# Performance work log

Measured on AMD Instinct MI355X. Metric: run time of the kernel, lower is better.

## Reference

```python
import jax, jax.numpy as jnp
import numpy as np

H = 256      # hidden_dim
D = 64       # dim_dynamic
ND = 2       # num_dynamic
PR = 7       # pooler_resolution
S = PR * PR  # 49 spatial positions
B = 4800     # N * nr_boxes
P = H * D    # num_params
EPS = 1e-5


def setup_inputs() -> dict:
    key = jax.random.key(0)
    ks = jax.random.split(key, 32)
    def w(k, shape):
        return jax.random.normal(k, shape, dtype=jnp.float32) * 0.02
    inp = {
        "pro_features": jax.random.normal(ks[0], (1, B, H), jnp.float32),
        "roi_features": jax.random.normal(ks[1], (S, B, H), jnp.float32),
        "pos_xywh": jax.random.normal(ks[2], (1, B, H), jnp.float32),
        "pos_img": jax.random.normal(ks[3], (S, B, H), jnp.float32),
        "pos_local": jax.random.uniform(ks[4], (PR, PR), jnp.float32),
        "bboxes_xywh": jax.random.uniform(ks[5], (B, 4), jnp.float32, minval=0.2, maxval=1.0),
        # dynamic_layer: H -> ND*P
        "Wd": w(ks[6], (H, ND * P)), "bd": jnp.zeros((ND * P,), jnp.float32),
        # query_scale MLP (2 layers, H->H->H)
        "Wqs1": w(ks[7], (H, H)), "bqs1": jnp.zeros((H,), jnp.float32),
        "Wqs2": w(ks[8], (H, H)), "bqs2": jnp.zeros((H,), jnp.float32),
        # ref_point_head MLP (2 layers, H->H->2)
        "Wr1": w(ks[9], (H, H)), "br1": jnp.zeros((H,), jnp.float32),
        "Wr2": w(ks[10], (H, 2)), "br2": jnp.zeros((2,), jnp.float32),
        # ca_qpos_proj / ca_kpos_proj
        "Wq": w(ks[11], (H, H)), "bq": jnp.zeros((H,), jnp.float32),
        "Wk": w(ks[12], (H, H)), "bk": jnp.zeros((H,), jnp.float32),
        # layer norms
        "g1": jnp.ones((D,), jnp.float32), "be1": jnp.zeros((D,), jnp.float32),
        "g2": jnp.ones((H,), jnp.float32), "be2": jnp.zeros((H,), jnp.float32),
        "g3": jnp.ones((H,), jnp.float32), "be3": jnp.zeros((H,), jnp.float32),
        # out_layer: (H*S) -> H
        "Wo": w(ks[13], (H * S, H)), "bo": jnp.zeros((H,), jnp.float32),
    }
    return inp


def _ln(x, g, b):
    m = jnp.mean(x, axis=-1, keepdims=True)
    v = jnp.mean((x - m) ** 2, axis=-1, keepdims=True)
    return (x - m) * jax.lax.rsqrt(v + EPS) * g + b


def reference(pro_features, roi_features, pos_xywh, pos_img, pos_local, bboxes_xywh,
              Wd, bd, Wqs1, bqs1, Wqs2, bqs2, Wr1, br1, Wr2, br2,
              Wq, bq, Wk, bk, g1, be1, g2, be2, g3, be3, Wo, bo):
    # (S,B,H) -> (B,S,H)
    features_pos = jnp.transpose(pos_img @ Wq + bq, (1, 0, 2))
    features = jnp.transpose(roi_features, (1, 0, 2))
    # dynamic parameters: (1,B,ND*P) -> (B,1,ND*P)
    parameters = jnp.transpose(pro_features @ Wd + bd, (1, 0, 2))
    # query_scale MLP
    pos_t = jax.nn.relu(pro_features @ Wqs1 + bqs1) @ Wqs2 + bqs2  # (1,B,H)
    px = pos_xywh[..., :H] * pos_t                                 # (1,B,H)
    # ref_point_head -> sigmoid
    ref = jax.nn.sigmoid(jax.nn.relu(pro_features @ Wr1 + br1) @ Wr2 + br2)  # (1,B,2)
    bb = bboxes_xywh.reshape(1, -1, 4)
    hi = px[..., H // 2:] * (ref[..., 0] / bb[..., 2])[..., None]
    lo = px[..., :H // 2] * (ref[..., 1] / bb[..., 3])[..., None]
    px = jnp.concatenate([lo, hi], axis=-1)
    # (B,1,H) * (1,S,1) -> (B,S,H)
    px = jnp.transpose(px, (1, 0, 2)) * pos_local.reshape(-1)[None, :, None]
    param1_pos = px @ Wk + bk                                      # (B,S,H)
    param1 = parameters[:, :, :P].reshape(-1, H, D)                # (B,H,D)
    param2 = parameters[:, :, P:].reshape(-1, D, H)                # (B,D,H)
    f = jnp.einsum('bsh,bhd->bsd', features, param1)               # (B,S,D)
    fp = jnp.sum(features_pos * param1_pos, axis=-1)               # (B,S)
    f = f + fp[:, :, None]
    f = jax.nn.relu(_ln(f, g1, be1))
    f = jnp.einsum('bsd,bdh->bsh', f, param2)                      # (B,S,H)
    f = jax.nn.relu(_ln(f, g2, be2))
    f = f.reshape(f.shape[0], -1) @ Wo + bo                        # (B,H)
    f = jax.nn.relu(_ln(f, g3, be3))
    return f
```

## Files before the change

### kernel.cpp

```cpp
#include <hip/hip_runtime.h>
#include <hip/hip_bf16.h>

#define HH 256
#define DD 64
#define SS 49
#define BB 4800
#define PP 16384
#define NDP 32768
#define KWO 12544
#define MPAD 4864
#define SK 8
#define KCH 1568

typedef unsigned int u32;
typedef unsigned short u16;
typedef __attribute__((ext_vector_type(8))) short bf16x8;
typedef __attribute__((ext_vector_type(4))) float f32x4;

__device__ __forceinline__ float bf2f(__hip_bfloat16 h) { return __bfloat162float(h); }

__device__ __forceinline__ void load_lds16(const void* g, void* l) {
  __builtin_amdgcn_global_load_lds(
      (const __attribute__((address_space(1))) unsigned int*)g,
      (__attribute__((address_space(3))) unsigned int*)l, 16, 0, 0);
}

__device__ __forceinline__ int nperm(int n) {
  if (n < PP) { int h = n >> 6, d = n & 63; return d * HH + h; }
  int r = n - PP; int d = r >> 8, h = r & 255; return PP + h * DD + d;
}

__device__ __forceinline__ float wave_sum64(float v) {
#pragma unroll
  for (int off = 32; off > 0; off >>= 1) v += __shfl_xor(v, off);
  return v;
}

__device__ __forceinline__ float block_sum256(float v, float* red) {
  v = wave_sum64(v);
  int w = threadIdx.x >> 6;
  if ((threadIdx.x & 63) == 0) red[w] = v;
  __syncthreads();
  float r = red[0] + red[1] + red[2] + red[3];
  __syncthreads();
  return r;
}

__global__ void k0_prep(const float* __restrict__ Wq, const float* __restrict__ bk,
                        const float* __restrict__ bq, float* __restrict__ w2c2) {
  __shared__ float red[4];
  int k = blockIdx.x, h = threadIdx.x;
  float v = Wq[k * HH + h];
  float s = block_sum256(v * bk[h], red);
  if (h == 0) w2c2[k] = s;
  if (k == 0) {
    float s2 = block_sum256(bq[h] * bk[h], red);
    if (h == 0) w2c2[HH] = s2;
  }
}

__global__ __launch_bounds__(256) void kc_w1(
    const float* __restrict__ Wqs1, const float* __restrict__ Wqs2,
    const float* __restrict__ Wr1, const float* __restrict__ Wk,
    const float* __restrict__ Wq,
    u16* __restrict__ w1t, u16* __restrict__ w2t, u16* __restrict__ wr1t,
    u16* __restrict__ wkt, u16* __restrict__ wqh) {
  int t = threadIdx.x;
  int zi = blockIdx.z;
  if (zi == 4) {
    int row = blockIdx.y * 32 + (t >> 3), col = blockIdx.x * 32 + (t & 7) * 4;
    float4 v = *(const float4*)&Wq[row * HH + col];
    union { u16 u[4]; uint2 q; } pk;
    __hip_bfloat16 hb;
    hb = __float2bfloat16(v.x); pk.u[0] = *(u16*)&hb;
    hb = __float2bfloat16(v.y); pk.u[1] = *(u16*)&hb;
    hb = __float2bfloat16(v.z); pk.u[2] = *(u16*)&hb;
    hb = __float2bfloat16(v.w); pk.u[3] = *(u16*)&hb;
    *(uint2*)&wqh[row * HH + col] = pk.q;
    return;
  }
  const float* src = (zi == 0) ? Wqs1 : (zi == 1) ? Wqs2 : (zi == 2) ? Wr1 : Wk;
  u16* dst = (zi == 0) ? w1t : (zi == 1) ? w2t : (zi == 2) ? wr1t : wkt;
  __shared__ float tile[32][33];
  int n0 = blockIdx.x * 32, k0 = blockIdx.y * 32;
  {
    int kk = t >> 3, nn = (t & 7) * 4;
    float4 v = *(const float4*)&src[(k0 + kk) * HH + n0 + nn];
    tile[kk][nn + 0] = v.x;
    tile[kk][nn + 1] = v.y;
    tile[kk][nn + 2] = v.z;
    tile[kk][nn + 3] = v.w;
  }
  __syncthreads();
  {
    int nn = t >> 3, kk = (t & 7) * 4;
    union { u16 u[4]; uint2 q; } pk;
#pragma unroll
    for (int i = 0; i < 4; ++i) {
      __hip_bfloat16 hb = __float2bfloat16(tile[kk + i][nn]);
      pk.u[i] = *(u16*)&hb;
    }
    *(uint2*)&dst[(n0 + nn) * HH + k0 + kk] = pk.q;
  }
}

__device__ __forceinline__ void g_gemm(const u16* aLb, const u16* __restrict__ Bg,
                                       int wm, int wn, int lg, int lr,
                                       f32x4 acc[2][4]) {
#pragma unroll
  for (int k0 = 0; k0 < HH; k0 += 32) {
    int colb = (k0 + (lg << 3)) << 1;
    bf16x8 af[2];
#pragma unroll
    for (int mi = 0; mi < 2; ++mi) {
      int row = wm * 32 + mi * 16 + lr;
      af[mi] = *(const bf16x8*)((const char*)aLb + (row << 9) +
                                (colb ^ ((row & 7) << 4)));
    }
    bf16x8 bfr[4];
#pragma unroll
    for (int ni = 0; ni < 4; ++ni) {
      int n = wn * 64 + ni * 16 + lr;
      bfr[ni] = *(const bf16x8*)&Bg[n * HH + k0 + (lg << 3)];
    }
#pragma unroll
    for (int mi = 0; mi < 2; ++mi)
#pragma unroll
      for (int ni = 0; ni < 4; ++ni)
        acc[mi][ni] = __builtin_amdgcn_mfma_f32_16x16x32_bf16(af[mi], bfr[ni], acc[mi][ni], 0, 0, 0);
  }
}

__device__ __forceinline__ void c_write(u16* xLb, f32x4 acc[2][4],
                                        const float* __restrict__ bias, bool dorelu,
                                        int wm, int wn, int lg, int lr) {
#pragma unroll
  for (int ni = 0; ni < 4; ++ni) {
    int col = wn * 64 + ni * 16 + lr;
    float bv = bias ? bias[col] : 0.f;
#pragma unroll
    for (int mi = 0; mi < 2; ++mi) {
#pragma unroll
      for (int j = 0; j < 4; ++j) {
        int row = wm * 32 + mi * 16 + (lg << 2) + j;
        float v = acc[mi][ni][j] + bv;
        if (dorelu) v = fmaxf(v, 0.f);
        __hip_bfloat16 hb = __float2bfloat16(v);
        *(u16*)((char*)xLb + (row << 9) + (((col << 1)) ^ ((row & 7) << 4))) = *(u16*)&hb;
      }
    }
  }
}

__global__ __launch_bounds__(512) void k1_mfma(
    const u16* __restrict__ proh, const float* __restrict__ posx,
    const float* __restrict__ bbox,
    const u16* __restrict__ w1t, const u16* __restrict__ w2t,
    const u16* __restrict__ wr1t, const u16* __restrict__ wkt,
    const u16* __restrict__ wqh,
    const float* __restrict__ bqs1, const float* __restrict__ bqs2,
    const float* __restrict__ br1, const float* __restrict__ Wr2,
    const float* __restrict__ br2, const float* __restrict__ bq,
    float* __restrict__ z, float* __restrict__ c1) {
  __shared__ u16 aL[16384];
  __shared__ u16 xL[16384];
  __shared__ float red0[512], red1[512];
  __shared__ float scLoL[64], scHiL[64];
  const int t = threadIdx.x;
  const int w = t >> 6, l = t & 63;
  const int lg = l >> 4, lr = l & 15;
  const int wm = w >> 2, wn = w & 3;
  const int m0 = blockIdx.x * 64;

#pragma unroll
  for (int i = 0; i < 4; ++i) {
    int c = i * 512 + t;
    int a = c * 16;
    int row = a >> 9, x0 = a & 511;
    int src = (m0 + row) * HH + ((x0 ^ ((row & 7) << 4)) >> 1);
    load_lds16(proh + src, (char*)aL + (size_t)(i * 512 + (w << 6)) * 16);
  }
  __syncthreads();

  {
    f32x4 acc[2][4] = {};
    g_gemm(aL, wr1t, wm, wn, lg, lr, acc);
    c_write(xL, acc, br1, true, wm, wn, lg, lr);
  }
  __syncthreads();
  {
    int row = t & 63, seg = t >> 6;
    float s0 = 0.f, s1 = 0.f;
#pragma unroll 8
    for (int hh = 0; hh < 32; ++hh) {
      int h = seg * 32 + hh;
      float rv = bf2f(*(const __hip_bfloat16*)((const char*)xL + (row << 9) +
                                               (((h << 1)) ^ ((row & 7) << 4))));
      s0 = fmaf(rv, Wr2[h * 2 + 0], s0);
      s1 = fmaf(rv, Wr2[h * 2 + 1], s1);
    }
    red0[row * 8 + seg] = s0;
    red1[row * 8 + seg] = s1;
  }
  __syncthreads();
  if (t < 64) {
    float s0 = br2[0], s1 = br2[1];
#pragma unroll
    for (int k = 0; k < 8; ++k) {
      s0 += red0[t * 8 + k];
      s1 += red1[t * 8 + k];
    }
    float r0 = 1.f / (1.f + __expf(-s0));
    float r1 = 1.f / (1.f + __expf(-s1));
    scHiL[t] = r0 / bbox[(m0 + t) * 4 + 2];
    scLoL[t] = r1 / bbox[(m0 + t) * 4 + 3];
  }
  f32x4 acc1[2][4] = {};
  g_gemm(aL, w1t, wm, wn, lg, lr, acc1);
  __syncthreads();
  c_write(xL, acc1, bqs1, true, wm, wn, lg, lr);
  __syncthreads();
  f32x4 accp[2][4] = {};
  g_gemm(xL, w2t, wm, wn, lg, lr, accp);
  __syncthreads();
#pragma unroll
  for (int ni = 0; ni < 4; ++ni) {
    int col = wn * 64 + ni * 16 + lr;
    float bv = bqs2[col];
#pragma unroll
    for (int mi = 0; mi < 2; ++mi) {
#pragma unroll
      for (int j = 0; j < 4; ++j) {
        int row = wm * 32 + mi * 16 + (lg << 2) + j;
        float pt = accp[mi][ni][j] + bv;
        float sc = (col < 128) ? scLoL[row] : scHiL[row];
        float v = posx[(m0 + row) * HH + col] * pt * sc;
        __hip_bfloat16 hb = __float2bfloat16(v);
        *(u16*)((char*)aL + (row << 9) + (((col << 1)) ^ ((row & 7) << 4))) = *(u16*)&hb;
      }
    }
  }
  __syncthreads();
  {
    f32x4 acc[2][4] = {};
    g_gemm(aL, wkt, wm, wn, lg, lr, acc);
    c_write(xL, acc, nullptr, false, wm, wn, lg, lr);
  }
  __syncthreads();
  {
    int row = t & 63, seg = t >> 6;
    float s0 = 0.f;
#pragma unroll 8
    for (int hh = 0; hh < 32; ++hh) {
      int h = seg * 32 + hh;
      float yv = bf2f(*(const __hip_bfloat16*)((const char*)xL + (row << 9) +
                                               (((h << 1)) ^ ((row & 7) << 4))));
      s0 = fmaf(yv, bq[h], s0);
    }
    red0[row * 8 + seg] = s0;
  }
  f32x4 accz[2][4] = {};
  g_gemm(xL, wqh, wm, wn, lg, lr, accz);
  __syncthreads();
  if (t < 64) {
    float s = 0.f;
#pragma unroll
    for (int k = 0; k < 8; ++k) s += red0[t * 8 + k];
    c1[m0 + t] = s;
  }
#pragma unroll
  for (int ni = 0; ni < 4; ++ni) {
    int col = wn * 64 + ni * 16 + lr;
#pragma unroll
    for (int mi = 0; mi < 2; ++mi) {
#pragma unroll
      for (int j = 0; j < 4; ++j) {
        int row = wm * 32 + mi * 16 + (lg << 2) + j;
        z[(size_t)(m0 + row) * HH + col] = accz[mi][ni][j];
      }
    }
  }
}

__global__ __launch_bounds__(256) void k2_fp(
    const float* __restrict__ posi, const float* __restrict__ posl,
    const float* __restrict__ z, const float* __restrict__ c1,
    const float* __restrict__ w2c2, float* __restrict__ fp) {
  int b = blockIdx.x, t = threadIdx.x;
  int l = t & 63, w = t >> 6;
  float4 zv = *(const float4*)&z[b * HH + l * 4];
  float4 wv = *(const float4*)&w2c2[l * 4];
  float c1b = c1[b];
  float c2 = w2c2[HH];
  for (int s = w; s < SS; s += 4) {
    float4 pi = *(const float4*)&posi[((size_t)s * BB + b) * HH + l * 4];
    float d1 = pi.x * zv.x + pi.y * zv.y + pi.z * zv.z + pi.w * zv.w;
    float d2 = pi.x * wv.x + pi.y * wv.y + pi.z * wv.z + pi.w * wv.w;
#pragma unroll
    for (int off = 32; off > 0; off >>= 1) {
      d1 += __shfl_xor(d1, off);
      d2 += __shfl_xor(d2, off);
    }
    if (l == 0) fp[b * SS + s] = posl[s] * (d1 + c1b) + d2 + c2;
  }
}

__global__ __launch_bounds__(256) void kc_pro(const float* __restrict__ pro,
                                              u16* __restrict__ proh) {
  int tg = blockIdx.x * 256 + threadIdx.x;
  int e0 = tg * 8;
  int row = e0 >> 8;
  union { u16 u[8]; uint4 v; } pk;
  if (row < BB) {
    float4 v0 = *(const float4*)&pro[e0];
    float4 v1 = *(const float4*)&pro[e0 + 4];
    float vv[8] = {v0.x, v0.y, v0.z, v0.w, v1.x, v1.y, v1.z, v1.w};
#pragma unroll
    for (int i = 0; i < 8; ++i) {
      __hip_bfloat16 hb = __float2bfloat16(vv[i]);
      pk.u[i] = *(u16*)&hb;
    }
  } else {
    pk.v = make_uint4(0, 0, 0, 0);
  }
  *(uint4*)&proh[e0] = pk.v;
}

__global__ __launch_bounds__(256) void kc_wdt(const float* __restrict__ Wd,
                                              u16* __restrict__ wdt) {
  __shared__ float tile[32][33];
  int n0 = blockIdx.x * 32;
  int k0 = blockIdx.y * 32;
  int t = threadIdx.x;
  {
    int kk = t >> 3, nn = (t & 7) * 4;
    float4 v = *(const float4*)&Wd[(size_t)(k0 + kk) * NDP + n0 + nn];
    tile[kk][nn + 0] = v.x;
    tile[kk][nn + 1] = v.y;
    tile[kk][nn + 2] = v.z;
    tile[kk][nn + 3] = v.w;
  }
  __syncthreads();
  {
    int nn = t >> 3, kk = (t & 7) * 4;
    union { u16 u[4]; uint2 v; } pk;
#pragma unroll
    for (int i = 0; i < 4; ++i) {
      __hip_bfloat16 hb = __float2bfloat16(tile[kk + i][nn]);
      pk.u[i] = *(u16*)&hb;
    }
    int np = nperm(n0 + nn);
    *(uint2*)&wdt[(size_t)np * HH + k0 + kk] = pk.v;
  }
}

__global__ void kc_bdp(const float* __restrict__ bd, float* __restrict__ bdp) {
  int n = blockIdx.x * 256 + threadIdx.x;
  bdp[nperm(n)] = bd[n];
}

__global__ __launch_bounds__(256) void kc_wot(const float* __restrict__ Wo,
                                              u16* __restrict__ wot) {
  __shared__ float tile[32][33];
  int k0 = blockIdx.x * 32;
  int n0 = blockIdx.y * 32;
  int t = threadIdx.x;
  {
    int kk = t >> 3, nn = (t & 7) * 4;
    float4 v = *(const float4*)&Wo[(size_t)(k0 + kk) * HH + n0 + nn];
    tile[kk][nn + 0] = v.x;
    tile[kk][nn + 1] = v.y;
    tile[kk][nn + 2] = v.z;
    tile[kk][nn + 3] = v.w;
  }
  __syncthreads();
  {
    int nn = t >> 3, kk = (t & 7) * 4;
    union { u16 u[4]; uint2 v; } pk;
#pragma unroll
    for (int i = 0; i < 4; ++i) {
      __hip_bfloat16 hb = __float2bfloat16(tile[kk + i][nn]);
      pk.u[i] = *(u16*)&hb;
    }
    *(uint2*)&wot[(size_t)(n0 + nn) * KWO + k0 + kk] = pk.v;
  }
}

__global__ __launch_bounds__(256) void k3_mfma(const u16* __restrict__ proh,
                                               const u16* __restrict__ wdt,
                                               const float* __restrict__ bdp,
                                               u16* __restrict__ params) {
  __shared__ char smem[32768];
  u16* Al = (u16*)smem;
  u16* Bl = (u16*)(smem + 8192);
  const int t = threadIdx.x;
  const int w = t >> 6, l = t & 63;
  const int n0 = blockIdx.x * 128;
  const int m0 = blockIdx.y * 128;
  const int wr = w >> 1, wc = w & 1;
  f32x4 acc[4][4] = {};

  for (int k0 = 0; k0 < HH; k0 += 32) {
#pragma unroll
    for (int i = 0; i < 2; ++i) {
      int c = i * 256 + t;
      int r = c >> 2, kq = (c & 3) * 8;
      int wbase = (i * 256 + (w << 6)) * 8;
      load_lds16(proh + (size_t)(m0 + r) * HH + k0 + kq, Al + wbase);
      load_lds16(wdt + (size_t)(n0 + r) * HH + k0 + kq, Bl + wbase);
    }
    __syncthreads();
    bf16x8 af[4], bfr[4];
#pragma unroll
    for (int mi = 0; mi < 4; ++mi)
      af[mi] = *(const bf16x8*)&Al[(wr * 64 + mi * 16 + (l & 15)) * 32 + (l >> 4) * 8];
#pragma unroll
    for (int ni = 0; ni < 4; ++ni)
      bfr[ni] = *(const bf16x8*)&Bl[(wc * 64 + ni * 16 + (l & 15)) * 32 + (l >> 4) * 8];
#pragma unroll
    for (int mi = 0; mi < 4; ++mi)
#pragma unroll
      for (int ni = 0; ni < 4; ++ni)
        acc[mi][ni] = __builtin_amdgcn_mfma_f32_16x16x32_bf16(af[mi], bfr[ni], acc[mi][ni], 0, 0, 0);
    __syncthreads();
  }
  u16* cb = (u16*)smem;
#pragma unroll
  for (int ni = 0; ni < 4; ++ni) {
    int col = wc * 64 + ni * 16 + (l & 15);
    float bias = bdp[n0 + col];
#pragma unroll
    for (int mi = 0; mi < 4; ++mi) {
#pragma unroll
      for (int j = 0; j < 4; ++j) {
        int row = wr * 64 + mi * 16 + ((l >> 4) << 2) + j;
        __hip_bfloat16 hb = __float2bfloat16(acc[mi][ni][j] + bias);
        cb[row * 128 + col] = *(u16*)&hb;
      }
    }
  }
  __syncthreads();
#pragma unroll
  for (int i = 0; i < 8; ++i) {
    int idx = i * 256 + t;
    int row = idx >> 4, cc = (idx & 15) * 8;
    if (m0 + row < BB)
      *(uint4*)&params[(size_t)(m0 + row) * NDP + n0 + cc] = *(const uint4*)&cb[row * 128 + cc];
  }
}

__global__ __launch_bounds__(256) void k4_mfma(
    const float* __restrict__ roi, const u16* __restrict__ params,
    const float* __restrict__ fpbuf,
    const float* __restrict__ g1, const float* __restrict__ be1,
    const float* __restrict__ g2, const float* __restrict__ be2,
    u16* __restrict__ f2ws) {
  __shared__ u16 bufP1[16384];
  __shared__ u16 bufF[8192];
  __shared__ float fpL[64];
  __shared__ float g1L[64], b1L[64], g2L[256], b2L[256];

  const int b = blockIdx.x;
  const int t = threadIdx.x;
  const int w = t >> 6, l = t & 63;
  const int lg = l >> 4, lr = l & 15;
  const u16* p1g = params + (size_t)b * NDP;
  const u16* p2g = params + (size_t)b * NDP + PP;

#pragma unroll
  for (int i = 0; i < 8; ++i) {
    int c = i * 256 + t;
    int a = c * 16;
    int row = a >> 9, x0 = a & 511;
    load_lds16(p1g + row * HH + ((x0 ^ ((row & 7) << 4)) >> 1),
               (char*)bufP1 + (size_t)(i * 256 + (w << 6)) * 16);
  }
#pragma unroll
  for (int i = 0; i < 8; ++i) {
    int idx = i * 256 + t;
    int row = idx >> 5, c4 = (idx & 31) << 2;
    union { u16 u[4]; unsigned long long v; } pk;
    if (row < SS) {
      float4 v = *(const float4*)&roi[((size_t)row * BB + b) * HH + c4];
      __hip_bfloat16 h0 = __float2bfloat16(v.x), h1 = __float2bfloat16(v.y);
      __hip_bfloat16 h2 = __float2bfloat16(v.z), h3 = __float2bfloat16(v.w);
      pk.u[0] = *(u16*)&h0; pk.u[1] = *(u16*)&h1;
      pk.u[2] = *(u16*)&h2; pk.u[3] = *(u16*)&h3;
    } else {
      pk.v = 0ull;
    }
    int ab = (row << 8) + (((c4 << 1)) ^ ((row & 7) << 4));
    *(unsigned long long*)((char*)bufF + ab) = pk.v;
  }
  if (t < 64) {
    fpL[t] = (t < SS) ? fpbuf[b * SS + t] : 0.f;
    g1L[t] = g1[t];
    b1L[t] = be1[t];
  }
  g2L[t] = g2[t];
  b2L[t] = be2[t];
  __syncthreads();

  f32x4 acc1[4] = {};
#pragma unroll
  for (int k0 = 0; k0 < 128; k0 += 32) {
    int arow = w * 16 + lr;
    const bf16x8 af = *(const bf16x8*)((const char*)bufF + (arow << 8) +
                                       ((((k0 + (lg << 3)) << 1)) ^ ((arow & 7) << 4)));
    bf16x8 bfr[4];
#pragma unroll
    for (int ni = 0; ni < 4; ++ni) {
      int brow = ni * 16 + lr;
      bfr[ni] = *(const bf16x8*)((const char*)bufP1 + (brow << 9) +
                                 ((((k0 + (lg << 3)) << 1)) ^ ((brow & 7) << 4)));
    }
#pragma unroll
    for (int ni = 0; ni < 4; ++ni)
      acc1[ni] = __builtin_amdgcn_mfma_f32_16x16x32_bf16(af, bfr[ni], acc1[ni], 0, 0, 0);
  }
  __syncthreads();
#pragma unroll
  for (int i = 0; i < 8; ++i) {
    int idx = i * 256 + t;
    int row = idx >> 5, c4 = (idx & 31) << 2;
    union { u16 u[4]; unsigned long long v; } pk;
    if (row < SS) {
      float4 v = *(const float4*)&roi[((size_t)row * BB + b) * HH + 128 + c4];
      __hip_bfloat16 h0 = __float2bfloat16(v.x), h1 = __float2bfloat16(v.y);
      __hip_bfloat16 h2 = __float2bfloat16(v.z), h3 = __float2bfloat16(v.w);
      pk.u[0] = *(u16*)&h0; pk.u[1] = *(u16*)&h1;
      pk.u[2] = *(u16*)&h2; pk.u[3] = *(u16*)&h3;
    } else {
      pk.v = 0ull;
    }
    int ab = (row << 8) + (((c4 << 1)) ^ ((row & 7) << 4));
    *(unsigned long long*)((char*)bufF + ab) = pk.v;
  }
  __syncthreads();
#pragma unroll
  for (int k0 = 0; k0 < 128; k0 += 32) {
    int arow = w * 16 + lr;
    const bf16x8 af = *(const bf16x8*)((const char*)bufF + (arow << 8) +
                                       ((((k0 + (lg << 3)) << 1)) ^ ((arow & 7) << 4)));
    bf16x8 bfr[4];
#pragma unroll
    for (int ni = 0; ni < 4; ++ni) {
      int brow = ni * 16 + lr;
      bfr[ni] = *(const bf16x8*)((const char*)bufP1 + (brow << 9) +
                                 ((((128 + k0 + (lg << 3)) << 1)) ^ ((brow & 7) << 4)));
    }
#pragma unroll
    for (int ni = 0; ni < 4; ++ni)
      acc1[ni] = __builtin_amdgcn_mfma_f32_16x16x32_bf16(af, bfr[ni], acc1[ni], 0, 0, 0);
  }
  __syncthreads();

#pragma unroll
  for (int i = 0; i < 8; ++i) {
    int c = i * 256 + t;
    int a = c * 16;
    int row = a >> 7, x0 = a & 127;
    load_lds16(p2g + row * DD + ((x0 ^ ((row & 7) << 4)) >> 1),
               (char*)bufP1 + (size_t)(i * 256 + (w << 6)) * 16);
  }

  u16* f1L = bufF;
#pragma unroll
  for (int j = 0; j < 4; ++j) {
    int s = w * 16 + (lg << 2) + j;
    float fpv = fpL[s];
    float x[4], sum = 0.f, sq = 0.f;
#pragma unroll
    for (int ni = 0; ni < 4; ++ni) {
      x[ni] = acc1[ni][j] + fpv;
      sum += x[ni];
      sq += x[ni] * x[ni];
    }
#pragma unroll
    for (int off = 1; off < 16; off <<= 1) {
      sum += __shfl_xor(sum, off);
      sq += __shfl_xor(sq, off);
    }
    float m = sum * (1.f / 64.f);
    float rs = rsqrtf(sq * (1.f / 64.f) - m * m + 1e-5f);
#pragma unroll
    for (int ni = 0; ni < 4; ++ni) {
      int d = ni * 16 + lr;
      float o = fmaxf((x[ni] - m) * rs * g1L[d] + b1L[d], 0.f);
      __hip_bfloat16 hb = __float2bfloat16(o);
      *(u16*)((char*)f1L + (s << 7) + ((d << 1) ^ ((s & 7) << 4))) = *(u16*)&hb;
    }
  }
  __syncthreads();

  f32x4 acc2[16] = {};
#pragma unroll
  for (int k0 = 0; k0 < 64; k0 += 32) {
    int arow = w * 16 + lr;
    const bf16x8 af = *(const bf16x8*)((const char*)f1L + (arow << 7) +
                                       ((((k0 + (lg << 3)) << 1)) ^ ((arow & 7) << 4)));
#pragma unroll
    for (int ni = 0; ni < 16; ++ni) {
      int brow = ni * 16 + lr;
      const bf16x8 bfr = *(const bf16x8*)((const char*)bufP1 + (brow << 7) +
                                          ((((k0 + (lg << 3)) << 1)) ^ ((brow & 7) << 4)));
      acc2[ni] = __builtin_amdgcn_mfma_f32_16x16x32_bf16(af, bfr, acc2[ni], 0, 0, 0);
    }
  }

#pragma unroll
  for (int j = 0; j < 4; ++j) {
    int s = w * 16 + (lg << 2) + j;
    float sum = 0.f, sq = 0.f;
#pragma unroll
    for (int ni = 0; ni < 16; ++ni) {
      float v = acc2[ni][j];
      sum += v;
      sq += v * v;
    }
#pragma unroll
    for (int off = 1; off < 16; off <<= 1) {
      sum += __shfl_xor(sum, off);
      sq += __shfl_xor(sq, off);
    }
    float m = sum * (1.f / 256.f);
    float rs = rsqrtf(sq * (1.f / 256.f) - m * m + 1e-5f);
    if (s < SS) {
#pragma unroll
      for (int ni = 0; ni < 16; ++ni) {
        int h = ni * 16 + lr;
        float o = fmaxf((acc2[ni][j] - m) * rs * g2L[h] + b2L[h], 0.f);
        __hip_bfloat16 hb = __float2bfloat16(o);
        f2ws[(size_t)b * KWO + s * HH + h] = *(u16*)&hb;
      }
    }
  }
}

__global__ __launch_bounds__(256) void k5_mfma(const u16* __restrict__ f2,
                                               const u16* __restrict__ wot,
                                               float* __restrict__ part) {
  __shared__ char smem[12288];
  u16* Al = (u16*)smem;
  u16* Bl = (u16*)(smem + 4096);
  const int t = threadIdx.x;
  const int w = t >> 6, l = t & 63;
  const int sk = blockIdx.x;
  const int m0 = blockIdx.y * 64;
  const int n0 = blockIdx.z * 128;
  const size_t kbase = (size_t)sk * KCH;
  const int wr = w >> 1, wc = w & 1;
  f32x4 acc[2][4] = {};

  for (int k0 = 0; k0 < KCH; k0 += 32) {
    {
      int r = t >> 2, kq = (t & 3) * 8;
      int wbase = (w << 6) * 8;
      load_lds16(f2 + (size_t)(m0 + r) * KWO + kbase + k0 + kq, Al + wbase);
    }
#pragma unroll
    for (int i = 0; i < 2; ++i) {
      int c = i * 256 + t;
      int r = c >> 2, kq = (c & 3) * 8;
      int wbase = (i * 256 + (w << 6)) * 8;
      load_lds16(wot + (size_t)(n0 + r) * KWO + kbase + k0 + kq, Bl + wbase);
    }
    __syncthreads();
    bf16x8 af[2], bfr[4];
#pragma unroll
    for (int mi = 0; mi < 2; ++mi)
      af[mi] = *(const bf16x8*)&Al[(wr * 32 + mi * 16 + (l & 15)) * 32 + (l >> 4) * 8];
#pragma unroll
    for (int ni = 0; ni < 4; ++ni)
      bfr[ni] = *(const bf16x8*)&Bl[(wc * 64 + ni * 16 + (l & 15)) * 32 + (l >> 4) * 8];
#pragma unroll
    for (int mi = 0; mi < 2; ++mi)
#pragma unroll
      for (int ni = 0; ni < 4; ++ni)
        acc[mi][ni] = __builtin_amdgcn_mfma_f32_16x16x32_bf16(af[mi], bfr[ni], acc[mi][ni], 0, 0, 0);
    __syncthreads();
  }
#pragma unroll
  for (int mi = 0; mi < 2; ++mi) {
#pragma unroll
    for (int j = 0; j < 4; ++j) {
      int m = m0 + wr * 32 + mi * 16 + ((l >> 4) << 2) + j;
#pragma unroll
      for (int ni = 0; ni < 4; ++ni) {
        int n = n0 + wc * 64 + ni * 16 + (l & 15);
        part[((size_t)sk * BB + m) * HH + n] = acc[mi][ni][j];
      }
    }
  }
}

__global__ __launch_bounds__(256) void k5r_ln3(
    const float* __restrict__ part, const float* __restrict__ bo,
    const float* __restrict__ g3, const float* __restrict__ be3,
    float* __restrict__ out) {
  __shared__ float red[4];
  int b = blockIdx.x, t = threadIdx.x;
  float v = bo[t];
#pragma unroll
  for (int sk = 0; sk < SK; ++sk) v += part[((size_t)sk * BB + b) * HH + t];
  float m = block_sum256(v, red) * (1.f / HH);
  float d = v - m;
  float var = block_sum256(d * d, red) * (1.f / HH);
  out[b * HH + t] = fmaxf(fmaf(d * rsqrtf(var + 1e-5f), g3[t], be3[t]), 0.f);
}

extern "C" void kernel_launch(void* const* d_in, const int* in_sizes, int n_in,
                              void* d_out, int out_size, void* d_ws, size_t ws_size,
                              hipStream_t stream) {
  const float* pro  = (const float*)d_in[0];
  const float* roi  = (const float*)d_in[1];
  const float* posx = (const float*)d_in[2];
  const float* posi = (const float*)d_in[3];
  const float* posl = (const float*)d_in[4];
  const float* bbox = (const float*)d_in[5];
  const float* Wd   = (const float*)d_in[6];
  const float* bd   = (const float*)d_in[7];
  const float* Wqs1 = (const float*)d_in[8];
  const float* bqs1 = (const float*)d_in[9];
  const float* Wqs2 = (const float*)d_in[10];
  const float* bqs2 = (const float*)d_in[11];
  const float* Wr1  = (const float*)d_in[12];
  const float* br1  = (const float*)d_in[13];
  const float* Wr2  = (const float*)d_in[14];
  const float* br2  = (const float*)d_in[15];
  const float* Wq   = (const float*)d_in[16];
  const float* bq   = (const float*)d_in[17];
  const float* Wk   = (const float*)d_in[18];
  const float* bk   = (const float*)d_in[19];
  const float* g1   = (const float*)d_in[20];
  const float* be1  = (const float*)d_in[21];
  const float* g2   = (const float*)d_in[22];
  const float* be2  = (const float*)d_in[23];
  const float* g3   = (const float*)d_in[24];
  const float* be3  = (const float*)d_in[25];
  const float* Wo   = (const float*)d_in[26];
  const float* bo   = (const float*)d_in[27];

  char* ws = (char*)d_ws;
  u16* w1t  = (u16*)(ws + 0ull);
  u16* w2t  = (u16*)(ws + 131072ull);
  u16* wr1t = (u16*)(ws + 262144ull);
  u16* wkt  = (u16*)(ws + 393216ull);
  u16* wqh  = (u16*)(ws + 524288ull);
  u16* params = (u16*)(ws + 0ull);
  float* part = (float*)(ws + 0ull);
  u16* f2ws   = (u16*)(ws + 314572800ull);
  u16* proh   = (u16*)(ws + 314572800ull);
  u16* wdt    = (u16*)(ws + 317063168ull);
  float* z    = (float*)(ws + 434995200ull);
  u16* wot    = (u16*)(ws + 434995200ull);
  float* bdp  = (float*)(ws + 441417728ull);
  float* fp   = (float*)(ws + 444825600ull);
  float* c1   = (float*)(ws + 445766400ull);
  float* w2c2 = (float*)(ws + 446047744ull);

  kc_pro<<<dim3(MPAD * HH / 8 / 256), dim3(256), 0, stream>>>(pro, proh);
  kc_w1<<<dim3(8, 8, 5), dim3(256), 0, stream>>>(Wqs1, Wqs2, Wr1, Wk, Wq,
                                                 w1t, w2t, wr1t, wkt, wqh);
  k0_prep<<<dim3(256), dim3(256), 0, stream>>>(Wq, bk, bq, w2c2);
  k1_mfma<<<dim3(BB / 64), dim3(512), 0, stream>>>(proh, posx, bbox, w1t, w2t, wr1t,
                                                   wkt, wqh, bqs1, bqs2, br1, Wr2,
                                                   br2, bq, z, c1);
  k2_fp<<<dim3(BB), dim3(256), 0, stream>>>(posi, posl, z, c1, w2c2, fp);
  kc_wot<<<dim3(KWO / 32, HH / 32), dim3(256), 0, stream>>>(Wo, wot);
  kc_wdt<<<dim3(NDP / 32, HH / 32), dim3(256), 0, stream>>>(Wd, wdt);
  kc_bdp<<<dim3(NDP / 256), dim3(256), 0, stream>>>(bd, bdp);
  k3_mfma<<<dim3(NDP / 128, MPAD / 128), dim3(256), 0, stream>>>(proh, wdt, bdp, params);
  k4_mfma<<<dim3(BB), dim3(256), 0, stream>>>(roi, params, fp, g1, be1, g2, be2, f2ws);
  k5_mfma<<<dim3(SK, BB / 64, HH / 128), dim3(256), 0, stream>>>(f2ws, wot, part);
  k5r_ln3<<<dim3(BB), dim3(256), 0, stream>>>(part, bo, g3, be3, (float*)d_out);
}
```

Before: 534.3 us.

## Use 64-wide K tiles with XOR-swizzled LDS in GEMMs and halve k4 LDS footprint

The k3 and k5 GEMM kernels now stage 64-wide K tiles instead of 32, which halves the number of barrier pairs per K loop. Their LDS tiles use an XOR swizzle to avoid bank conflicts on the fragment reads. k4 now streams its per-box parameter matrices in two halves through a 16KB buffer instead of holding a 32KB one, cutting LDS use so more blocks can be resident, at the cost of extra barriers and reloads. The split-K count for the output GEMM changes from 8 to 7, giving fewer partial sums to reduce but less parallelism.

```diff
diff --git a/kernel.cpp b/kernel.cpp
--- a/kernel.cpp
+++ b/kernel.cpp
@@ -9,8 +9,8 @@
 #define NDP 32768
 #define KWO 12544
 #define MPAD 4864
-#define SK 8
-#define KCH 1568
+#define SK 7
+#define KCH 1792
 
 typedef unsigned int u32;
 typedef unsigned short u16;
@@ -392,48 +392,60 @@
                                                u16* __restrict__ params) {
   __shared__ char smem[32768];
   u16* Al = (u16*)smem;
-  u16* Bl = (u16*)(smem + 8192);
+  u16* Bl = (u16*)(smem + 16384);
   const int t = threadIdx.x;
   const int w = t >> 6, l = t & 63;
+  const int lg = l >> 4, lr = l & 15;
   const int n0 = blockIdx.x * 128;
   const int m0 = blockIdx.y * 128;
   const int wr = w >> 1, wc = w & 1;
   f32x4 acc[4][4] = {};
 
-  for (int k0 = 0; k0 < HH; k0 += 32) {
-#pragma unroll
-    for (int i = 0; i < 2; ++i) {
+  for (int k0 = 0; k0 < HH; k0 += 64) {
+#pragma unroll
+    for (int i = 0; i < 4; ++i) {
       int c = i * 256 + t;
-      int r = c >> 2, kq = (c & 3) * 8;
-      int wbase = (i * 256 + (w << 6)) * 8;
-      load_lds16(proh + (size_t)(m0 + r) * HH + k0 + kq, Al + wbase);
-      load_lds16(wdt + (size_t)(n0 + r) * HH + k0 + kq, Bl + wbase);
+      int row = c >> 3, x0 = (c & 7) * 16;
+      int koff = (x0 ^ ((row & 7) << 4)) >> 1;
+      load_lds16(proh + (size_t)(m0 + row) * HH + k0 + koff,
+                 (char*)Al + (size_t)(i * 256 + (w << 6)) * 16);
+      load_lds16(wdt + (size_t)(n0 + row) * HH + k0 + koff,
+                 (char*)Bl + (size_t)(i * 256 + (w << 6)) * 16);
     }
     __syncthreads();
-    bf16x8 af[4], bfr[4];
-#pragma unroll
-    for (int mi = 0; mi < 4; ++mi)
-      af[mi] = *(const bf16x8*)&Al[(wr * 64 + mi * 16 + (l & 15)) * 32 + (l >> 4) * 8];
-#pragma unroll
-    for (int ni = 0; ni < 4; ++ni)
-      bfr[ni] = *(const bf16x8*)&Bl[(wc * 64 + ni * 16 + (l & 15)) * 32 + (l >> 4) * 8];
-#pragma unroll
-    for (int mi = 0; mi < 4; ++mi)
-#pragma unroll
-      for (int ni = 0; ni < 4; ++ni)
-        acc[mi][ni] = __builtin_amdgcn_mfma_f32_16x16x32_bf16(af[mi], bfr[ni], acc[mi][ni], 0, 0, 0);
+#pragma unroll
+    for (int kk = 0; kk < 64; kk += 32) {
+      bf16x8 af[4], bfr[4];
+#pragma unroll
+      for (int mi = 0; mi < 4; ++mi) {
+        int row = wr * 64 + mi * 16 + lr;
+        af[mi] = *(const bf16x8*)((const char*)Al + (row << 7) +
+                                  ((((kk + (lg << 3)) << 1)) ^ ((row & 7) << 4)));
+      }
+#pragma unroll
+      for (int ni = 0; ni < 4; ++ni) {
+        int row = wc * 64 + ni * 16 + lr;
+        bfr[ni] = *(const bf16x8*)((const char*)Bl + (row << 7) +
+                                   ((((kk + (lg << 3)) << 1)) ^ ((row & 7) << 4)));
+      }
+#pragma unroll
+      for (int mi = 0; mi < 4; ++mi)
+#pragma unroll
+        for (int ni = 0; ni < 4; ++ni)
+          acc[mi][ni] = __builtin_amdgcn_mfma_f32_16x16x32_bf16(af[mi], bfr[ni], acc[mi][ni], 0, 0, 0);
+    }
     __syncthreads();
   }
   u16* cb = (u16*)smem;
 #pragma unroll
   for (int ni = 0; ni < 4; ++ni) {
-    int col = wc * 64 + ni * 16 + (l & 15);
+    int col = wc * 64 + ni * 16 + lr;
     float bias = bdp[n0 + col];
 #pragma unroll
     for (int mi = 0; mi < 4; ++mi) {
 #pragma unroll
       for (int j = 0; j < 4; ++j) {
-        int row = wr * 64 + mi * 16 + ((l >> 4) << 2) + j;
+        int row = wr * 64 + mi * 16 + (lg << 2) + j;
         __hip_bfloat16 hb = __float2bfloat16(acc[mi][ni][j] + bias);
         cb[row * 128 + col] = *(u16*)&hb;
       }
@@ -455,7 +467,7 @@
     const float* __restrict__ g1, const float* __restrict__ be1,
     const float* __restrict__ g2, const float* __restrict__ be2,
     u16* __restrict__ f2ws) {
-  __shared__ u16 bufP1[16384];
+  __shared__ u16 bufP[8192];
   __shared__ u16 bufF[8192];
   __shared__ float fpL[64];
   __shared__ float g1L[64], b1L[64], g2L[256], b2L[256];
@@ -467,101 +479,69 @@
   const u16* p1g = params + (size_t)b * NDP;
   const u16* p2g = params + (size_t)b * NDP + PP;
 
-#pragma unroll
-  for (int i = 0; i < 8; ++i) {
+  f32x4 acc1[4] = {};
+#pragma unroll
+  for (int half = 0; half < 2; ++half) {
+    const int hoff = half * 128;
+#pragma unroll
+    for (int i = 0; i < 4; ++i) {
+      int c = i * 256 + t;
+      int row = c >> 4, x0 = (c & 15) * 16;
+      load_lds16(p1g + row * HH + hoff + ((x0 ^ ((row & 7) << 4)) >> 1),
+                 (char*)bufP + (size_t)(i * 256 + (w << 6)) * 16);
+    }
+#pragma unroll
+    for (int i = 0; i < 8; ++i) {
+      int idx = i * 256 + t;
+      int row = idx >> 5, c4 = (idx & 31) << 2;
+      union { u16 u[4]; unsigned long long v; } pk;
+      if (row < SS) {
+        float4 v = *(const float4*)&roi[((size_t)row * BB + b) * HH + hoff + c4];
+        __hip_bfloat16 h0 = __float2bfloat16(v.x), h1 = __float2bfloat16(v.y);
+        __hip_bfloat16 h2 = __float2bfloat16(v.z), h3 = __float2bfloat16(v.w);
+        pk.u[0] = *(u16*)&h0; pk.u[1] = *(u16*)&h1;
+        pk.u[2] = *(u16*)&h2; pk.u[3] = *(u16*)&h3;
+      } else {
+        pk.v = 0ull;
+      }
+      int ab = (row << 8) + (((c4 << 1)) ^ ((row & 7) << 4));
+      *(unsigned long long*)((char*)bufF + ab) = pk.v;
+    }
+    if (half == 0) {
+      if (t < 64) {
+        fpL[t] = (t < SS) ? fpbuf[b * SS + t] : 0.f;
+        g1L[t] = g1[t];
+        b1L[t] = be1[t];
+      }
+      g2L[t] = g2[t];
+      b2L[t] = be2[t];
+    }
+    __syncthreads();
+#pragma unroll
+    for (int kk = 0; kk < 128; kk += 32) {
+      int arow = w * 16 + lr;
+      const bf16x8 af = *(const bf16x8*)((const char*)bufF + (arow << 8) +
+                                         ((((kk + (lg << 3)) << 1)) ^ ((arow & 7) << 4)));
+      bf16x8 bfr[4];
+#pragma unroll
+      for (int ni = 0; ni < 4; ++ni) {
+        int brow = ni * 16 + lr;
+        bfr[ni] = *(const bf16x8*)((const char*)bufP + (brow << 8) +
+                                   ((((kk + (lg << 3)) << 1)) ^ ((brow & 7) << 4)));
+      }
+#pragma unroll
+      for (int ni = 0; ni < 4; ++ni)
+        acc1[ni] = __builtin_amdgcn_mfma_f32_16x16x32_bf16(af, bfr[ni], acc1[ni], 0, 0, 0);
+    }
+    __syncthreads();
+  }
+
+#pragma unroll
+  for (int i = 0; i < 4; ++i) {
     int c = i * 256 + t;
-    int a = c * 16;
-    int row = a >> 9, x0 = a & 511;
-    load_lds16(p1g + row * HH + ((x0 ^ ((row & 7) << 4)) >> 1),
-               (char*)bufP1 + (size_t)(i * 256 + (w << 6)) * 16);
-  }
-#pragma unroll
-  for (int i = 0; i < 8; ++i) {
-    int idx = i * 256 + t;
-    int row = idx >> 5, c4 = (idx & 31) << 2;
-    union { u16 u[4]; unsigned long long v; } pk;
-    if (row < SS) {
-      float4 v = *(const float4*)&roi[((size_t)row * BB + b) * HH + c4];
-      __hip_bfloat16 h0 = __float2bfloat16(v.x), h1 = __float2bfloat16(v.y);
-      __hip_bfloat16 h2 = __float2bfloat16(v.z), h3 = __float2bfloat16(v.w);
-      pk.u[0] = *(u16*)&h0; pk.u[1] = *(u16*)&h1;
-      pk.u[2] = *(u16*)&h2; pk.u[3] = *(u16*)&h3;
-    } else {
-      pk.v = 0ull;
-    }
-    int ab = (row << 8) + (((c4 << 1)) ^ ((row & 7) << 4));
-    *(unsigned long long*)((char*)bufF + ab) = pk.v;
-  }
-  if (t < 64) {
-    fpL[t] = (t < SS) ? fpbuf[b * SS + t] : 0.f;
-    g1L[t] = g1[t];
-    b1L[t] = be1[t];
-  }
-  g2L[t] = g2[t];
-  b2L[t] = be2[t];
-  __syncthreads();
-
-  f32x4 acc1[4] = {};
-#pragma unroll
-  for (int k0 = 0; k0 < 128; k0 += 32) {
-    int arow = w * 16 + lr;
-    const bf16x8 af = *(const bf16x8*)((const char*)bufF + (arow << 8) +
-                                       ((((k0 + (lg << 3)) << 1)) ^ ((arow & 7) << 4)));
-    bf16x8 bfr[4];
-#pragma unroll
-    for (int ni = 0; ni < 4; ++ni) {
-      int brow = ni * 16 + lr;
-      bfr[ni] = *(const bf16x8*)((const char*)bufP1 + (brow << 9) +
-                                 ((((k0 + (lg << 3)) << 1)) ^ ((brow & 7) << 4)));
-    }
-#pragma unroll
-    for (int ni = 0; ni < 4; ++ni)
-      acc1[ni] = __builtin_amdgcn_mfma_f32_16x16x32_bf16(af, bfr[ni], acc1[ni], 0, 0, 0);
-  }
-  __syncthreads();
-#pragma unroll
-  for (int i = 0; i < 8; ++i) {
-    int idx = i * 256 + t;
-    int row = idx >> 5, c4 = (idx & 31) << 2;
-    union { u16 u[4]; unsigned long long v; } pk;
-    if (row < SS) {
-      float4 v = *(const float4*)&roi[((size_t)row * BB + b) * HH + 128 + c4];
-      __hip_bfloat16 h0 = __float2bfloat16(v.x), h1 = __float2bfloat16(v.y);
-      __hip_bfloat16 h2 = __float2bfloat16(v.z), h3 = __float2bfloat16(v.w);
-      pk.u[0] = *(u16*)&h0; pk.u[1] = *(u16*)&h1;
-      pk.u[2] = *(u16*)&h2; pk.u[3] = *(u16*)&h3;
-    } else {
-      pk.v = 0ull;
-    }
-    int ab = (row << 8) + (((c4 << 1)) ^ ((row & 7) << 4));
-    *(unsigned long long*)((char*)bufF + ab) = pk.v;
-  }
-  __syncthreads();
-#pragma unroll
-  for (int k0 = 0; k0 < 128; k0 += 32) {
-    int arow = w * 16 + lr;
-    const bf16x8 af = *(const bf16x8*)((const char*)bufF + (arow << 8) +
-                                       ((((k0 + (lg << 3)) << 1)) ^ ((arow & 7) << 4)));
-    bf16x8 bfr[4];
-#pragma unroll
-    for (int ni = 0; ni < 4; ++ni) {
-      int brow = ni * 16 + lr;
-      bfr[ni] = *(const bf16x8*)((const char*)bufP1 + (brow << 9) +
-                                 ((((128 + k0 + (lg << 3)) << 1)) ^ ((brow & 7) << 4)));
-    }
-#pragma unroll
-    for (int ni = 0; ni < 4; ++ni)
-      acc1[ni] = __builtin_amdgcn_mfma_f32_16x16x32_bf16(af, bfr[ni], acc1[ni], 0, 0, 0);
-  }
-  __syncthreads();
-
-#pragma unroll
-  for (int i = 0; i < 8; ++i) {
-    int c = i * 256 + t;
-    int a = c * 16;
-    int row = a >> 7, x0 = a & 127;
+    int row = c >> 3, x0 = (c & 7) * 16;
     load_lds16(p2g + row * DD + ((x0 ^ ((row & 7) << 4)) >> 1),
-               (char*)bufP1 + (size_t)(i * 256 + (w << 6)) * 16);
+               (char*)bufP + (size_t)(i * 256 + (w << 6)) * 16);
   }
 
   u16* f1L = bufF;
@@ -595,16 +575,30 @@
 
   f32x4 acc2[16] = {};
 #pragma unroll
-  for (int k0 = 0; k0 < 64; k0 += 32) {
-    int arow = w * 16 + lr;
-    const bf16x8 af = *(const bf16x8*)((const char*)f1L + (arow << 7) +
-                                       ((((k0 + (lg << 3)) << 1)) ^ ((arow & 7) << 4)));
-#pragma unroll
-    for (int ni = 0; ni < 16; ++ni) {
-      int brow = ni * 16 + lr;
-      const bf16x8 bfr = *(const bf16x8*)((const char*)bufP1 + (brow << 7) +
-                                          ((((k0 + (lg << 3)) << 1)) ^ ((brow & 7) << 4)));
-      acc2[ni] = __builtin_amdgcn_mfma_f32_16x16x32_bf16(af, bfr, acc2[ni], 0, 0, 0);
+  for (int nh = 0; nh < 2; ++nh) {
+    if (nh == 1) {
+      __syncthreads();
+#pragma unroll
+      for (int i = 0; i < 4; ++i) {
+        int c = i * 256 + t;
+        int row = c >> 3, x0 = (c & 7) * 16;
+        load_lds16(p2g + (128 + row) * DD + ((x0 ^ ((row & 7) << 4)) >> 1),
+                   (char*)bufP + (size_t)(i * 256 + (w << 6)) * 16);
+      }
+      __syncthreads();
+    }
+#pragma unroll
+    for (int kk = 0; kk < 64; kk += 32) {
+      int arow = w * 16 + lr;
+      const bf16x8 af = *(const bf16x8*)((const char*)f1L + (arow << 7) +
+                                         ((((kk + (lg << 3)) << 1)) ^ ((arow & 7) << 4)));
+#pragma unroll
+      for (int ni = 0; ni < 8; ++ni) {
+        int brow = ni * 16 + lr;
+        const bf16x8 bfr = *(const bf16x8*)((const char*)bufP + (brow << 7) +
+                                            ((((kk + (lg << 3)) << 1)) ^ ((brow & 7) << 4)));
+        acc2[nh * 8 + ni] = __builtin_amdgcn_mfma_f32_16x16x32_bf16(af, bfr, acc2[nh * 8 + ni], 0, 0, 0);
+      }
     }
   }
 
@@ -640,11 +634,12 @@
 __global__ __launch_bounds__(256) void k5_mfma(const u16* __restrict__ f2,
                                                const u16* __restrict__ wot,
                                                float* __restrict__ part) {
-  __shared__ char smem[12288];
+  __shared__ char smem[24576];
   u16* Al = (u16*)smem;
-  u16* Bl = (u16*)(smem + 4096);
+  u16* Bl = (u16*)(smem + 8192);
   const int t = threadIdx.x;
   const int w = t >> 6, l = t & 63;
+  const int lg = l >> 4, lr = l & 15;
   const int sk = blockIdx.x;
   const int m0 = blockIdx.y * 64;
   const int n0 = blockIdx.z * 128;
@@ -652,32 +647,43 @@
   const int wr = w >> 1, wc = w & 1;
   f32x4 acc[2][4] = {};
 
-  for (int k0 = 0; k0 < KCH; k0 += 32) {
-    {
-      int r = t >> 2, kq = (t & 3) * 8;
-      int wbase = (w << 6) * 8;
-      load_lds16(f2 + (size_t)(m0 + r) * KWO + kbase + k0 + kq, Al + wbase);
-    }
+  for (int k0 = 0; k0 < KCH; k0 += 64) {
 #pragma unroll
     for (int i = 0; i < 2; ++i) {
       int c = i * 256 + t;
-      int r = c >> 2, kq = (c & 3) * 8;
-      int wbase = (i * 256 + (w << 6)) * 8;
-      load_lds16(wot + (size_t)(n0 + r) * KWO + kbase + k0 + kq, Bl + wbase);
+      int row = c >> 3, x0 = (c & 7) * 16;
+      load_lds16(f2 + (size_t)(m0 + row) * KWO + kbase + k0 + ((x0 ^ ((row & 7) << 4)) >> 1),
+                 (char*)Al + (size_t)(i * 256 + (w << 6)) * 16);
+    }
+#pragma unroll
+    for (int i = 0; i < 4; ++i) {
+      int c = i * 256 + t;
+      int row = c >> 3, x0 = (c & 7) * 16;
+      load_lds16(wot + (size_t)(n0 + row) * KWO + kbase + k0 + ((x0 ^ ((row & 7) << 4)) >> 1),
+                 (char*)Bl + (size_t)(i * 256 + (w << 6)) * 16);
     }
     __syncthreads();
-    bf16x8 af[2], bfr[4];
-#pragma unroll
-    for (int mi = 0; mi < 2; ++mi)
-      af[mi] = *(const bf16x8*)&Al[(wr * 32 + mi * 16 + (l & 15)) * 32 + (l >> 4) * 8];
-#pragma unroll
-    for (int ni = 0; ni < 4; ++ni)
-      bfr[ni] = *(const bf16x8*)&Bl[(wc * 64 + ni * 16 + (l & 15)) * 32 + (l >> 4) * 8];
-#pragma unroll
-    for (int mi = 0; mi < 2; ++mi)
-#pragma unroll
-      for (int ni = 0; ni < 4; ++ni)
-        acc[mi][ni] = __builtin_amdgcn_mfma_f32_16x16x32_bf16(af[mi], bfr[ni], acc[mi][ni], 0, 0, 0);
+#pragma unroll
+    for (int kk = 0; kk < 64; kk += 32) {
+      bf16x8 af[2], bfr[4];
+#pragma unroll
+      for (int mi = 0; mi < 2; ++mi) {
+        int row = wr * 32 + mi * 16 + lr;
+        af[mi] = *(const bf16x8*)((const char*)Al + (row << 7) +
+                                  ((((kk + (lg << 3)) << 1)) ^ ((row & 7) << 4)));
+      }
+#pragma unroll
+      for (int ni = 0; ni < 4; ++ni) {
+        int row = wc * 64 + ni * 16 + lr;
+        bfr[ni] = *(const bf16x8*)((const char*)Bl + (row << 7) +
+                                   ((((kk + (lg << 3)) << 1)) ^ ((row & 7) << 4)));
+      }
+#pragma unroll
+      for (int mi = 0; mi < 2; ++mi)
+#pragma unroll
+        for (int ni = 0; ni < 4; ++ni)
+          acc[mi][ni] = __builtin_amdgcn_mfma_f32_16x16x32_bf16(af[mi], bfr[ni], acc[mi][ni], 0, 0, 0);
+    }
     __syncthreads();
   }
 #pragma unroll
```

Measured after the change: 548.9 us. +2.7%, slower.
